# Kernel optimization log

Measured on AMD Instinct MI355X. Metric: run time of the kernel, lower is better.

The kernel has to match this reference:

```python
import jax, jax.numpy as jnp
import numpy as np

B, T, C, H = 8, 1024, 768, 12
D = C // H  # head_dim = 64


def setup_inputs() -> dict:
    key = jax.random.key(0)
    ks = jax.random.split(key, 5)
    return {
        "x": jax.random.normal(ks[0], (B, T, C), dtype=jnp.float32),
        "W_in": jax.random.normal(ks[1], (C, 3 * C), dtype=jnp.float32) * 0.02,
        "b_in": jax.random.normal(ks[2], (3 * C,), dtype=jnp.float32) * 0.02,
        "W_out": jax.random.normal(ks[3], (C, C), dtype=jnp.float32) * 0.02,
        "b_out": jax.random.normal(ks[4], (C,), dtype=jnp.float32) * 0.02,
    }


def reference(x, W_in, b_in, W_out, b_out):
    b, t, c = x.shape
    qkv = x @ W_in + b_in                       # [b, t, 3c]
    # NOTE: original code splits as (k, q, v) -- k first!
    k, q, v = jnp.split(qkv, 3, axis=2)
    # [b, h, t, d]
    k = k.reshape(b, t, H, D).transpose(0, 2, 1, 3)
    q = q.reshape(b, t, H, D).transpose(0, 2, 1, 3)
    v = v.reshape(b, t, H, D).transpose(0, 2, 1, 3)
    # NOTE: original applies NO 1/sqrt(d) scaling.
    scores = jnp.einsum("bhqd,bhkd->bhqk", q, k)
    causal = jnp.tril(jnp.ones((t, t), dtype=bool))
    scores = jnp.where(causal[None, None], scores, -jnp.inf)
    attn = jax.nn.softmax(scores, axis=-1)
    y = jnp.einsum("bhqk,bhkd->bhqd", attn, v)  # [b, h, t, d]
    y = y.transpose(0, 2, 1, 3).reshape(b, t, c)
    return y @ W_out + b_out
```

## Files before the change

### kernel.cpp

```cpp
#include <hip/hip_runtime.h>
#include <hip/hip_bf16.h>
#include <stdint.h>


typedef __bf16 bf16;
typedef __attribute__((ext_vector_type(4))) __bf16 bf16x4;
typedef __attribute__((ext_vector_type(8))) __bf16 bf16x8;
typedef __attribute__((ext_vector_type(4))) float f32x4;

#define NB 8
#define NT 1024
#define NC 768
#define NH 12
#define ND 64
#define NM (NB*NT)
#define N3C (3*NC)

typedef __attribute__((address_space(1))) void as1_void;
typedef __attribute__((address_space(3))) void as3_void;

__device__ __forceinline__ void gload_lds16(const void* g, void* l) {
  __builtin_amdgcn_global_load_lds((as1_void*)g, (as3_void*)l, 16, 0, 0);
}


__global__ void k_convert(const float* __restrict__ src, bf16* __restrict__ dst, int n4) {
  int i = blockIdx.x * blockDim.x + threadIdx.x;
  if (i < n4) {
    float4 v = reinterpret_cast<const float4*>(src)[i];
    bf16x4 o = { (bf16)v.x, (bf16)v.y, (bf16)v.z, (bf16)v.w };
    reinterpret_cast<bf16x4*>(dst)[i] = o;
  }
}

__global__ void k_transpose_w(const float* __restrict__ src, bf16* __restrict__ dst,
                              int R, int C) {
  __shared__ float tile[32][33];
  const int c0 = blockIdx.x * 32, r0 = blockIdx.y * 32;
  const int tx = threadIdx.x & 31, ty = threadIdx.x >> 5;
#pragma unroll
  for (int i = 0; i < 4; i++)
    tile[ty + i*8][tx] = src[(size_t)(r0 + ty + i*8) * C + c0 + tx];
  __syncthreads();
#pragma unroll
  for (int i = 0; i < 4; i++)
    dst[(size_t)(c0 + ty + i*8) * R + r0 + tx] = (bf16)tile[tx][ty + i*8];
}

template<int MODE, int TM>
__global__ void __launch_bounds__(256, (TM == 128 ? 2 : 3))
k_gemm_bt(const bf16* __restrict__ A, const bf16* __restrict__ Bt,
          const float* __restrict__ bias, float* __restrict__ Cout,
          bf16* __restrict__ qp, bf16* __restrict__ kp,
          bf16* __restrict__ vp,
          int M, int N, int K) {
  constexpr int MF  = TM / 32;
  constexpr int WM  = TM / 2;
  constexpr int NLD = MF + 4;
  __shared__ __align__(16) bf16 As[2][TM*64];
  __shared__ __align__(16) bf16 Bs[2][128*64];

  const int gx = gridDim.x;
  int lin = blockIdx.y * gx + blockIdx.x;
  const int cpx = (gx * gridDim.y) >> 3;
  lin = (lin & 7) * cpx + (lin >> 3);
  const int tm = (lin % gx) * TM, tn = (lin / gx) * 128;

  const int tid = threadIdx.x, lane = tid & 63, w = tid >> 6;
  const int wr = w >> 1, wc = w & 1;
  const int lr = lane & 15, lhi = lane >> 4;
  const int rsw = lr & 7;
  const int sr = tid >> 3;
  const int sc = ((tid & 7) ^ (sr & 7)) * 8;
  const int nk = K / 64;

  auto stage = [&](bf16* as, bf16* bs, int kt) {
#pragma unroll
    for (int ch = 0; ch < MF; ch++)
      gload_lds16(A + (size_t)(tm + ch*32 + sr) * K + kt + sc,
                  (char*)as + ch*4096 + tid*16);
#pragma unroll
    for (int ch = 0; ch < 4; ch++)
      gload_lds16(Bt + (size_t)(tn + ch*32 + sr) * K + kt + sc,
                  (char*)bs + ch*4096 + tid*16);
  };

  f32x4 acc[MF][4];
#pragma unroll
  for (int m = 0; m < MF; m++)
#pragma unroll
    for (int n = 0; n < 4; n++) acc[m][n] = (f32x4){0.f, 0.f, 0.f, 0.f};

  stage(As[0], Bs[0], 0);
  int cur = 0;

  for (int t = 0; t < nk; ++t) {
    const int ktn = (t + 1 < nk ? t + 1 : t) * 64;
    stage(As[cur ^ 1], Bs[cur ^ 1], ktn);
    asm volatile("s_waitcnt vmcnt(%0)" :: "i"(NLD) : "memory");
    __builtin_amdgcn_s_barrier();

    const char* a0 = (const char*)As[cur];
    const char* b0 = (const char*)Bs[cur];
#pragma unroll
    for (int kk = 0; kk < 2; kk++) {
      bf16x8 af[MF], bfr[4];
#pragma unroll
      for (int m = 0; m < MF; m++)
        af[m] = *reinterpret_cast<const bf16x8*>(
            a0 + (wr*WM + m*16 + lr) * 128 + (((kk*4 + lhi) ^ rsw) << 4));
#pragma unroll
      for (int n = 0; n < 4; n++)
        bfr[n] = *reinterpret_cast<const bf16x8*>(
            b0 + (wc*64 + n*16 + lr) * 128 + (((kk*4 + lhi) ^ rsw) << 4));
#pragma unroll
      for (int m = 0; m < MF; m++)
#pragma unroll
        for (int n = 0; n < 4; n++)
          acc[m][n] = __builtin_amdgcn_mfma_f32_16x16x32_bf16(af[m], bfr[n], acc[m][n], 0, 0, 0);
    }

    asm volatile("s_waitcnt lgkmcnt(0)" ::: "memory");
    __builtin_amdgcn_sched_barrier(0);
    __builtin_amdgcn_s_barrier();
    cur ^= 1;
  }
  asm volatile("s_waitcnt vmcnt(0)" ::: "memory");

  if (MODE == 0) {
#pragma unroll
    for (int m = 0; m < MF; m++)
#pragma unroll
      for (int n = 0; n < 4; n++) {
        const int col = tn + wc*64 + n*16 + lr;
        const float bv = bias[col];
#pragma unroll
        for (int j = 0; j < 4; j++) {
          const int row = tm + wr*WM + m*16 + lhi*4 + j;
          Cout[(size_t)row * N + col] = acc[m][n][j] + bv;
        }
      }
  } else {
    const int part = tn / NC;
#pragma unroll
    for (int m = 0; m < MF; m++)
#pragma unroll
      for (int n = 0; n < 4; n++) {
        const int col = tn + wc*64 + n*16 + lr;
        const float bv = bias[col];
        const int cp = col - part * NC;
        const int h = cp >> 6, d = cp & 63;
#pragma unroll
        for (int j = 0; j < 4; j++) {
          const int row = tm + wr*WM + m*16 + lhi*4 + j;
          const int b0i = row >> 10, t = row & 1023;
          const int bh = b0i * NH + h;
          const bf16 val = (bf16)(acc[m][n][j] + bv);
          if (part == 2) {
            const size_t idx =
                ((((size_t)bh*16 + (t>>6))*4 + (d>>4))*2 + ((t>>5)&1))*512
                + (size_t)((d&15) + ((t>>3)&3)*16)*8 + (t&7);
            vp[idx] = val;
          } else {
            const size_t idx =
                (((size_t)bh*64 + (t>>4))*2 + (d>>5))*512
                + (size_t)(((d>>3)&3)*16 + (t&15))*8 + (d&7);
            if (part == 0) kp[idx] = val; else qp[idx] = val;
          }
        }
      }
  }
}

__global__ void __launch_bounds__(64, 2)
k_attn(const bf16* __restrict__ qpack, const bf16* __restrict__ kpack,
       const bf16* __restrict__ vpack, bf16* __restrict__ y) {
  const int bh = blockIdx.x, b = bh / NH, h = bh % NH;
  const int p = blockIdx.y;
  const int lane = threadIdx.x;
  const int lr = lane & 15, lhi = lane >> 4;
  __shared__ __align__(16) bf16 P[32][68];

#define LOAD_K(DST, K0)                                                        \
  {                                                                            \
    _Pragma("unroll")                                                          \
    for (int g = 0; g < 4; g++)                                                \
      _Pragma("unroll")                                                        \
      for (int h2 = 0; h2 < 2; h2++)                                           \
        DST[g][h2] = *reinterpret_cast<const bf16x8*>(                         \
            kpack + (((size_t)bh*64 + ((K0)>>4) + g)*2 + h2)*512 + lane*8);    \
  }

#define ATTN_STEP(KCUR, KNXT, KB)                                              \
  {                                                                            \
    const int k0 = (KB) * 64;                                                  \
    const int kn = ((KB) + 1 < nkb) ? k0 + 64 : k0;                            \
                        \
    bf16x8 vf[4][2];                                                           \
    _Pragma("unroll")                                                          \
    for (int dg = 0; dg < 4; dg++)                                             \
      _Pragma("unroll")                                                        \
      for (int kk = 0; kk < 2; kk++)                                           \
        vf[dg][kk] = *reinterpret_cast<const bf16x8*>(                         \
            vpack + ((((size_t)bh*16 + (k0>>6))*4 + dg)*2 + kk)*512 + lane*8); \
                   \
    LOAD_K(KNXT, kn);                                                          \
    f32x4 S[2][4];                                                             \
    _Pragma("unroll")                                                          \
    for (int m = 0; m < 2; m++)                                                \
      _Pragma("unroll")                                                        \
      for (int g = 0; g < 4; g++) S[m][g] = (f32x4){0.f, 0.f, 0.f, 0.f};       \
    _Pragma("unroll")                                                          \
    for (int g = 0; g < 4; g++)                                                \
      _Pragma("unroll")                                                        \
      for (int m = 0; m < 2; m++) {                                            \
        S[m][g] = __builtin_amdgcn_mfma_f32_16x16x32_bf16(qf[m][0], KCUR[g][0],\
                                                          S[m][g], 0, 0, 0);   \
        S[m][g] = __builtin_amdgcn_mfma_f32_16x16x32_bf16(qf[m][1], KCUR[g][1],\
                                                          S[m][g], 0, 0, 0);   \
      }                                                                        \
    const bool need_mask = ((KB) == nkb - 1);                                  \
    _Pragma("unroll")                                                          \
    for (int m = 0; m < 2; m++)                                                \
      _Pragma("unroll")                                                        \
      for (int g = 0; g < 4; g++) {                                            \
        const int key = k0 + g*16 + lr;                                        \
        _Pragma("unroll")                                                      \
        for (int j = 0; j < 4; j++) {                                          \
          float s = S[m][g][j];                                                \
          if (need_mask) {                                                     \
            const int row = qbase + m*16 + lhi*4 + j;                          \
            if (key > row) s = -1e30f;                                         \
          }                                                                    \
          const float ppv = __expf(s);   \
          L[m][j] += ppv;                                                      \
          P[m*16 + lhi*4 + j][g*16 + lr] = (bf16)ppv;                          \
        }                                                                      \
      }                                                                        \
    _Pragma("unroll")                                                          \
    for (int m = 0; m < 2; m++)                                                \
      _Pragma("unroll")                                                        \
      for (int kk = 0; kk < 2; kk++) {                                         \
        bf16x8 pf = *reinterpret_cast<const bf16x8*>(&P[m*16 + lr][kk*32 + lhi*8]); \
        _Pragma("unroll")                                                      \
        for (int dg = 0; dg < 4; dg++)                                         \
          O[m][dg] = __builtin_amdgcn_mfma_f32_16x16x32_bf16(pf, vf[dg][kk],   \
                                                             O[m][dg], 0, 0, 0); \
      }                                                                        \
  }

#pragma unroll 1
  for (int half = 0; half < 2; half++) {
    const int qt = half ? (31 - p) : p;
    const int qbase = qt * 32;
    const int nkb = (qbase >> 6) + 1;

    bf16x8 qf[2][2];
#pragma unroll
    for (int m = 0; m < 2; m++)
#pragma unroll
      for (int kk = 0; kk < 2; kk++)
        qf[m][kk] = *reinterpret_cast<const bf16x8*>(
            qpack + (((size_t)bh*64 + (qbase>>4) + m)*2 + kk)*512 + lane*8);

    f32x4 O[2][4];
    float L[2][4];
#pragma unroll
    for (int m = 0; m < 2; m++) {
#pragma unroll
      for (int d = 0; d < 4; d++) O[m][d] = (f32x4){0.f, 0.f, 0.f, 0.f};
#pragma unroll
      for (int j = 0; j < 4; j++) L[m][j] = 0.f;
    }

    bf16x8 kfA[4][2], kfB[4][2];
    LOAD_K(kfA, 0);
    int kb = 0;
#pragma unroll 1
    while (true) {
      ATTN_STEP(kfA, kfB, kb);
      kb++;
      if (kb >= nkb) break;
      ATTN_STEP(kfB, kfA, kb);
      kb++;
      if (kb >= nkb) break;
    }

#pragma unroll
    for (int m = 0; m < 2; m++)
#pragma unroll
      for (int j = 0; j < 4; j++) {
        float l = L[m][j];
        l += __shfl_xor(l, 1);
        l += __shfl_xor(l, 2);
        l += __shfl_xor(l, 4);
        l += __shfl_xor(l, 8);
        L[m][j] = 1.0f / l;
      }

#pragma unroll
    for (int m = 0; m < 2; m++)
#pragma unroll
      for (int dg = 0; dg < 4; dg++)
#pragma unroll
        for (int j = 0; j < 4; j++) {
          const int row = qbase + m*16 + lhi*4 + j;
          const int col = h*ND + dg*16 + lr;
          y[(size_t)(b*NT + row) * NC + col] = (bf16)(O[m][dg][j] * L[m][j]);
        }
  }
#undef ATTN_STEP
#undef LOAD_K
}

extern "C" void kernel_launch(void* const* d_in, const int* in_sizes, int n_in,
                              void* d_out, int out_size, void* d_ws, size_t ws_size,
                              hipStream_t stream) {
  const float* x     = (const float*)d_in[0];
  const float* W_in  = (const float*)d_in[1];
  const float* b_in  = (const float*)d_in[2];
  const float* W_out = (const float*)d_in[3];
  const float* b_out = (const float*)d_in[4];
  float* out = (float*)d_out;
  char* ws = (char*)d_ws;

  bf16* xb    = (bf16*)(ws + 0);
  bf16* Wit   = (bf16*)(ws + 12582912);
  bf16* Wot   = (bf16*)(ws + 16121856);
  bf16* qpack = (bf16*)(ws + 17301504);
  bf16* kpack = (bf16*)(ws + 29884416);
  bf16* vpack = (bf16*)(ws + 42467328);

  k_convert<<<6144, 256, 0, stream>>>(x, xb, NM * NC / 4);
  k_transpose_w<<<dim3(N3C/32, NC/32), 256, 0, stream>>>(W_in, Wit, NC, N3C);
  k_transpose_w<<<dim3(NC/32, NC/32), 256, 0, stream>>>(W_out, Wot, NC, NC);

  k_gemm_bt<1,128><<<dim3(NM/128, N3C/128), 256, 0, stream>>>(
      xb, Wit, b_in, nullptr, qpack, kpack, vpack, NM, N3C, NC);

  k_attn<<<dim3(NB*NH, 16), 64, 0, stream>>>(qpack, kpack, vpack, xb );

  k_gemm_bt<0,64><<<dim3(NM/64, NC/128), 256, 0, stream>>>(
      xb, Wot, b_out, out, nullptr, nullptr, nullptr, NM, NC, NC);
}
```

Baseline: 204.3 us.

## Split attention key loop across two waves and drop GEMM XCD swizzle

The attention block grows to two waves, each handling alternating 64-key blocks with its own P buffer. Partial outputs and row sums are combined through LDS atomics, then normalized and written with vector stores. This aims to raise parallelism and occupancy in the small 64-thread attention kernel, at the cost of LDS atomics and extra barriers. Separately, the GEMM block index remapping that grouped tiles per XCD is removed in favor of direct blockIdx mapping, which may change L2 locality.

Measured after the change: 275.0 us. +34.6%, slower.

```diff
diff --git a/kernel.cpp b/kernel.cpp
--- a/kernel.cpp
+++ b/kernel.cpp
@@ -60,11 +60,7 @@
   __shared__ __align__(16) bf16 As[2][TM*64];
   __shared__ __align__(16) bf16 Bs[2][128*64];
 
-  const int gx = gridDim.x;
-  int lin = blockIdx.y * gx + blockIdx.x;
-  const int cpx = (gx * gridDim.y) >> 3;
-  lin = (lin & 7) * cpx + (lin >> 3);
-  const int tm = (lin % gx) * TM, tn = (lin / gx) * 128;
+  const int tm = blockIdx.x * TM, tn = blockIdx.y * 128;
 
   const int tid = threadIdx.x, lane = tid & 63, w = tid >> 6;
   const int wr = w >> 1, wc = w & 1;
@@ -172,14 +168,16 @@
   }
 }
 
-__global__ void __launch_bounds__(64, 2)
+__global__ void __launch_bounds__(128, 2)
 k_attn(const bf16* __restrict__ qpack, const bf16* __restrict__ kpack,
        const bf16* __restrict__ vpack, bf16* __restrict__ y) {
   const int bh = blockIdx.x, b = bh / NH, h = bh % NH;
   const int p = blockIdx.y;
-  const int lane = threadIdx.x;
+  const int tid = threadIdx.x, w = tid >> 6, lane = tid & 63;
   const int lr = lane & 15, lhi = lane >> 4;
-  __shared__ __align__(16) bf16 P[32][68];
+  __shared__ __align__(16) bf16 P[2][32][68];
+  __shared__ __align__(16) float Obuf[32][68];
+  __shared__ float Lbuf[32];
 
 #define LOAD_K(DST, K0)                                                        \
   {                                                                            \
@@ -194,7 +192,7 @@
 #define ATTN_STEP(KCUR, KNXT, KB)                                              \
   {                                                                            \
     const int k0 = (KB) * 64;                                                  \
-    const int kn = ((KB) + 1 < nkb) ? k0 + 64 : k0;                            \
+    const int kn = ((KB) + 2 < nkb) ? k0 + 128 : k0;                           \
                         \
     bf16x8 vf[4][2];                                                           \
     _Pragma("unroll")                                                          \
@@ -203,7 +201,7 @@
       for (int kk = 0; kk < 2; kk++)                                           \
         vf[dg][kk] = *reinterpret_cast<const bf16x8*>(                         \
             vpack + ((((size_t)bh*16 + (k0>>6))*4 + dg)*2 + kk)*512 + lane*8); \
-                   \
+                                  \
     LOAD_K(KNXT, kn);                                                          \
     f32x4 S[2][4];                                                             \
     _Pragma("unroll")                                                          \
@@ -234,14 +232,14 @@
           }                                                                    \
           const float ppv = __expf(s);   \
           L[m][j] += ppv;                                                      \
-          P[m*16 + lhi*4 + j][g*16 + lr] = (bf16)ppv;                          \
+          P[w][m*16 + lhi*4 + j][g*16 + lr] = (bf16)ppv;                       \
         }                                                                      \
       }                                                                        \
     _Pragma("unroll")                                                          \
     for (int m = 0; m < 2; m++)                                                \
       _Pragma("unroll")                                                        \
       for (int kk = 0; kk < 2; kk++) {                                         \
-        bf16x8 pf = *reinterpret_cast<const bf16x8*>(&P[m*16 + lr][kk*32 + lhi*8]); \
+        bf16x8 pf = *reinterpret_cast<const bf16x8*>(&P[w][m*16 + lr][kk*32 + lhi*8]); \
         _Pragma("unroll")                                                      \
         for (int dg = 0; dg < 4; dg++)                                         \
           O[m][dg] = __builtin_amdgcn_mfma_f32_16x16x32_bf16(pf, vf[dg][kk],   \
@@ -255,6 +253,10 @@
     const int qbase = qt * 32;
     const int nkb = (qbase >> 6) + 1;
 
+    for (int i = tid; i < 32*68; i += 128) ((float*)Obuf)[i] = 0.f;
+    if (tid < 32) Lbuf[tid] = 0.f;
+    __syncthreads();
+
     bf16x8 qf[2][2];
 #pragma unroll
     for (int m = 0; m < 2; m++)
@@ -274,16 +276,18 @@
     }
 
     bf16x8 kfA[4][2], kfB[4][2];
-    LOAD_K(kfA, 0);
-    int kb = 0;
+    LOAD_K(kfA, w*64);
+    int kb = w;
+    if (kb < nkb) {
 #pragma unroll 1
-    while (true) {
-      ATTN_STEP(kfA, kfB, kb);
-      kb++;
-      if (kb >= nkb) break;
-      ATTN_STEP(kfB, kfA, kb);
-      kb++;
-      if (kb >= nkb) break;
+      while (true) {
+        ATTN_STEP(kfA, kfB, kb);
+        kb += 2;
+        if (kb >= nkb) break;
+        ATTN_STEP(kfB, kfA, kb);
+        kb += 2;
+        if (kb >= nkb) break;
+      }
     }
 
 #pragma unroll
@@ -295,7 +299,7 @@
         l += __shfl_xor(l, 2);
         l += __shfl_xor(l, 4);
         l += __shfl_xor(l, 8);
-        L[m][j] = 1.0f / l;
+        L[m][j] = l;
       }
 
 #pragma unroll
@@ -303,11 +307,30 @@
 #pragma unroll
       for (int dg = 0; dg < 4; dg++)
 #pragma unroll
-        for (int j = 0; j < 4; j++) {
-          const int row = qbase + m*16 + lhi*4 + j;
-          const int col = h*ND + dg*16 + lr;
-          y[(size_t)(b*NT + row) * NC + col] = (bf16)(O[m][dg][j] * L[m][j]);
-        }
+        for (int j = 0; j < 4; j++)
+          atomicAdd(&Obuf[m*16 + lhi*4 + j][dg*16 + lr], O[m][dg][j]);
+    if (lr == 0)
+#pragma unroll
+      for (int m = 0; m < 2; m++)
+#pragma unroll
+        for (int j = 0; j < 4; j++)
+          atomicAdd(&Lbuf[m*16 + lhi*4 + j], L[m][j]);
+    __syncthreads();
+
+    {
+      const int q = tid >> 2, dvb = (tid & 3) * 16;
+      const float invl = 1.0f / Lbuf[q];
+      bf16x8 ov0, ov1;
+#pragma unroll
+      for (int i = 0; i < 8; i++) {
+        ov0[i] = (bf16)(Obuf[q][dvb + i] * invl);
+        ov1[i] = (bf16)(Obuf[q][dvb + 8 + i] * invl);
+      }
+      bf16* yp = y + (size_t)(b*NT + qbase + q) * NC + h*ND + dvb;
+      *reinterpret_cast<bf16x8*>(yp) = ov0;
+      *reinterpret_cast<bf16x8*>(yp + 8) = ov1;
+    }
+    __syncthreads();
   }
 #undef ATTN_STEP
 #undef LOAD_K
@@ -338,7 +361,7 @@
   k_gemm_bt<1,128><<<dim3(NM/128, N3C/128), 256, 0, stream>>>(
       xb, Wit, b_in, nullptr, qpack, kpack, vpack, NM, N3C, NC);
 
-  k_attn<<<dim3(NB*NH, 16), 64, 0, stream>>>(qpack, kpack, vpack, xb );
+  k_attn<<<dim3(NB*NH, 16), 128, 0, stream>>>(qpack, kpack, vpack, xb );
 
   k_gemm_bt<0,64><<<dim3(NM/64, NC/128), 256, 0, stream>>>(
       xb, Wot, b_out, out, nullptr, nullptr, nullptr, NM, NC, NC);
```
